# Kernel tuning notes

Measured on AMD Instinct MI355X. Metric: run time of the kernel, lower is better.

The kernel has to match this reference:

```python
import jax, jax.numpy as jnp
import numpy as np
from jax import lax

M_DIM = 128
L1 = L2 = L3 = L4 = 4
L = L1 * L2 * L3 * L4  # 256
RANK = 2
BATCH, D = 4, 16
W = D - RANK + 1  # 15 windows per dim (linear mode, stride 1, drop)


def _make_bbasis():
    # Bbasis[idx, i] = prod_d cos(2*pi*(j_d+1)/(i+2)), idx = ((j1*L2+j2)*L3+j3)*L4+j4
    i = jnp.arange(M_DIM, dtype=jnp.float32)
    def c(Ld):
        j = jnp.arange(D_ := Ld, dtype=jnp.float32)
        return jnp.cos(2.0 * jnp.pi * (j[:, None] + 1.0) / (i[None, :] + 2.0))  # (Ld, m)
    B1, B2, B3, B4 = c(L1), c(L2), c(L3), c(L4)
    Bb = (B1[:, None, None, None, :] * B2[None, :, None, None, :]
          * B3[None, None, :, None, :] * B4[None, None, None, :, :])
    return Bb.reshape(L, M_DIM).astype(jnp.float32)


def setup_inputs() -> dict:
    key = jax.random.key(0)
    k1, k2, k3 = jax.random.split(key, 3)
    vec_arr = jax.random.normal(k1, (BATCH, D, D, D, D, M_DIM), dtype=jnp.float32)
    # M initialized as identity + small noise (nn.init.eye_ is exactly eye; noise keeps grads non-trivial)
    M = jnp.eye(M_DIM, dtype=jnp.float32) + 0.01 * jax.random.normal(k2, (M_DIM, M_DIM), dtype=jnp.float32)
    Acoeff = jax.random.uniform(k3, (M_DIM, L), minval=-0.1, maxval=0.1, dtype=jnp.float32)
    Bbasis = _make_bbasis()
    return {"vec_arr": vec_arr, "M": M, "Acoeff": Acoeff, "Bbasis": Bbasis}


def _basis_index():
    # window coords k_d in [0, W), basis index uses j_d = k_d mod L_d
    k = jnp.arange(W)
    j1 = (k % L1)[:, None, None, None]
    j2 = (k % L2)[None, :, None, None]
    j3 = (k % L3)[None, None, :, None]
    j4 = (k % L4)[None, None, None, :]
    idx = ((j1 * L2 + j2) * L3 + j3) * L4 + j4  # (W,W,W,W)
    return idx.reshape(-1)  # (W^4,)


def reference(vec_arr, M, Acoeff, Bbasis):
    # 4D sliding-window mean (linear mode, stride 1, 'drop'), rank_op='avg'.
    # mean(window @ M.T) == mean(window) @ M.T (linearity), so pool then one GEMM.
    win = (1, RANK, RANK, RANK, RANK, 1)
    pooled = lax.reduce_window(vec_arr, jnp.float32(0.0), lax.add, win,
                               (1, 1, 1, 1, 1, 1), 'VALID') / float(RANK ** 4)
    # agg[b, k1..k4, j] = sum_i pooled[...,i] * M[j,i]  (i.e. x @ M.T)
    agg = jnp.einsum('bwxyzi,ji->bwxyzj', pooled, M)  # (B, W,W,W,W, m)
    agg = agg.reshape(agg.shape[0], -1, M_DIM)        # (B, W^4, m)
    idx = _basis_index()                               # (W^4,)
    # Position-dependent descriptor N(k) = Acoeff[:, idx] * Bbasis[idx, :]
    Nk = Acoeff.T[idx] * Bbasis[idx]                   # (W^4, m)
    return Nk[None, :, :] - agg                        # (B, W^4, m) deviation
```

## Files before the change

kernel.cpp:

```cpp
#include <hip/hip_runtime.h>
#include <hip/hip_bf16.h>
#include <stdint.h>

#define MD     128
#define W4     50625
#define ROWS   202500
#define LBAS   256
#define POOL_THREADS 432000
#define NK_OFF 51840000

typedef __attribute__((ext_vector_type(8))) __bf16 bf16x8;
typedef __attribute__((ext_vector_type(4))) float floatx4;
typedef __attribute__((ext_vector_type(8))) unsigned short ushortx8;
typedef __attribute__((ext_vector_type(4))) unsigned short ushortx4;

__device__ __forceinline__ float bf2f(unsigned short u){
  union { unsigned int i; float f; } v; v.i = ((unsigned int)u) << 16; return v.f;
}
__device__ __forceinline__ unsigned short f2bf(float x){
  union { float f; unsigned int i; } v; v.f = x;
  unsigned int r = v.i + 0x7FFFu + ((v.i >> 16) & 1u);
  return (unsigned short)(r >> 16);
}
__device__ __forceinline__ int detect_f32(const void* Bbasis){
  return ((const unsigned int*)Bbasis)[0] == 0x3F800000u;
}

__global__ __launch_bounds__(256) void nk_kernel(const void* __restrict__ Acoeff,
                                                 const void* __restrict__ Bbasis,
                                                 float* __restrict__ NkFull){
  int gid = blockIdx.x * 256 + threadIdx.x;
  if (gid >= LBAS * MD) return;
  int idx = gid >> 7;
  int j   = gid & 127;
  float a, b;
  if (detect_f32(Bbasis)){
    a = ((const float*)Acoeff)[j * LBAS + idx];
    b = ((const float*)Bbasis)[idx * MD + j];
  } else {
    a = bf2f(((const unsigned short*)Acoeff)[j * LBAS + idx]);
    b = bf2f(((const unsigned short*)Bbasis)[idx * MD + j]);
  }
  NkFull[gid] = a * b;
}

template<int ISF32>
__device__ __forceinline__ void pool_body(const void* __restrict__ vec,
                                          unsigned short* __restrict__ pooled,
                                          int gid){
  const int ig = gid & 31;
  unsigned int strip = (unsigned int)(gid >> 5);
  const unsigned int w4 = strip % 15u; strip /= 15u;
  const unsigned int w3 = strip % 15u; strip /= 15u;
  const unsigned int w2 = strip % 15u;
  const unsigned int b  = strip / 15u;
  const unsigned int base = b*8388608u + w2*32768u + w3*2048u + w4*128u
                          + (unsigned int)(ig * 4);
  unsigned int offs[8];
#pragma unroll
  for (int d = 0; d < 8; ++d){
    const unsigned int d2 = (d>>2)&1u, d3 = (d>>1)&1u, d4 = d&1u;
    offs[d] = base + d2*32768u + d3*2048u + d4*128u;
  }
  const unsigned int prowB = b*50625u + w2*225u + w3*15u + w4;
  float prev[4], cur[4];
#pragma unroll 4
  for (int k1 = 0; k1 < 16; ++k1){
#pragma unroll
    for (int e = 0; e < 4; ++e) cur[e] = 0.f;
#pragma unroll
    for (int d = 0; d < 8; ++d){
      const unsigned int off = offs[d] + (unsigned int)k1 * 524288u;
      if (ISF32){
        const floatx4 v = *(const floatx4*)((const float*)vec + off);
#pragma unroll
        for (int e = 0; e < 4; ++e) cur[e] += v[e];
      } else {
        const ushortx4 u = *(const ushortx4*)((const unsigned short*)vec + off);
#pragma unroll
        for (int e = 0; e < 4; ++e) cur[e] += bf2f(u[e]);
      }
    }
    if (k1 > 0){
      ushortx4 ov;
#pragma unroll
      for (int e = 0; e < 4; ++e) ov[e] = f2bf((prev[e] + cur[e]) * 0.0625f);
      *(ushortx4*)(pooled + (size_t)(prowB + (unsigned)(k1 - 1) * 3375u) * 128 + ig * 4) = ov;
    }
#pragma unroll
    for (int e = 0; e < 4; ++e) prev[e] = cur[e];
  }
}

__global__ __launch_bounds__(256) void pool_kernel(const void* __restrict__ vec,
                                                   const void* __restrict__ Bbasis,
                                                   unsigned short* __restrict__ pooled){
  int gid = blockIdx.x * 256 + threadIdx.x;
  if (gid >= POOL_THREADS) return;
  if (detect_f32(Bbasis)) pool_body<1>(vec, pooled, gid);
  else                    pool_body<0>(vec, pooled, gid);
}

union GemmSmem {
  struct { unsigned short A[128][136]; unsigned short B[128][136]; } ab;
  float C[128][132];
};

__global__ __launch_bounds__(256) void gemm_kernel(const unsigned short* __restrict__ pooled,
                                                   const void* __restrict__ Mmat,
                                                   const float* __restrict__ NkFull,
                                                   const void* __restrict__ Bbasis,
                                                   void* __restrict__ out){
  __shared__ __align__(16) GemmSmem sm;
  __shared__ int sIdx[128];

  const int tid = threadIdx.x;
  const int p0  = blockIdx.x * 128;
  const int isF32 = detect_f32(Bbasis);

  {
    const int rr  = tid >> 4;
    const int l16 = tid & 15;
#pragma unroll
    for (int r8 = 0; r8 < 8; ++r8){
      const int row = r8 * 16 + rr;
      *(ushortx8*)&sm.ab.A[row][l16 * 8] =
          *(const ushortx8*)(pooled + (size_t)(p0 + row) * 128 + l16 * 8);
    }
    if (isF32){
      const float* mf = (const float*)Mmat;
#pragma unroll
      for (int r8 = 0; r8 < 8; ++r8){
        const int row = r8 * 16 + rr;
        const float* src = mf + row * 128 + l16 * 8;
        floatx4 lo = *(const floatx4*)src;
        floatx4 hi = *(const floatx4*)(src + 4);
        ushortx8 v;
#pragma unroll
        for (int e = 0; e < 4; ++e){ v[e] = f2bf(lo[e]); v[4+e] = f2bf(hi[e]); }
        *(ushortx8*)&sm.ab.B[row][l16 * 8] = v;
      }
    } else {
      const unsigned short* mh = (const unsigned short*)Mmat;
#pragma unroll
      for (int r8 = 0; r8 < 8; ++r8){
        const int row = r8 * 16 + rr;
        *(ushortx8*)&sm.ab.B[row][l16 * 8] = *(const ushortx8*)(mh + row * 128 + l16 * 8);
      }
    }
  }
  if (tid < 128){
    const int p = p0 + tid;
    unsigned int w = (p < ROWS) ? (unsigned int)(p % W4) : 0u;
    const unsigned int w4 = w % 15u; w /= 15u;
    const unsigned int w3 = w % 15u; w /= 15u;
    const unsigned int w2 = w % 15u;
    const unsigned int w1 = w / 15u;
    sIdx[tid] = (int)(((w1 & 3u) << 6) | ((w2 & 3u) << 4) | ((w3 & 3u) << 2) | (w4 & 3u));
  }
  __syncthreads();

  const int wave = tid >> 6;
  const int lane = tid & 63;
  const int quad = lane >> 4;
  const int l16  = lane & 15;

  floatx4 acc[2][8];
#pragma unroll
  for (int rt = 0; rt < 2; ++rt)
#pragma unroll
    for (int c = 0; c < 8; ++c) acc[rt][c] = (floatx4){0.f, 0.f, 0.f, 0.f};

#pragma unroll
  for (int s = 0; s < 4; ++s){
    bf16x8 af[2];
#pragma unroll
    for (int rt = 0; rt < 2; ++rt)
      af[rt] = *(const bf16x8*)&sm.ab.A[wave * 32 + rt * 16 + l16][s * 32 + quad * 8];
#pragma unroll
    for (int c = 0; c < 8; ++c){
      const bf16x8 bfv = *(const bf16x8*)&sm.ab.B[c * 16 + l16][s * 32 + quad * 8];
      acc[0][c] = __builtin_amdgcn_mfma_f32_16x16x32_bf16(af[0], bfv, acc[0][c], 0, 0, 0);
      acc[1][c] = __builtin_amdgcn_mfma_f32_16x16x32_bf16(af[1], bfv, acc[1][c], 0, 0, 0);
    }
  }

  __syncthreads();
#pragma unroll
  for (int rt = 0; rt < 2; ++rt){
#pragma unroll
    for (int c = 0; c < 8; ++c){
#pragma unroll
      for (int reg = 0; reg < 4; ++reg){
        const int r = wave * 32 + rt * 16 + quad * 4 + reg;
        sm.C[r][c * 16 + l16] = acc[rt][c][reg];
      }
    }
  }
  __syncthreads();

  const int rsub = tid >> 5;
  const int col  = (tid & 31) * 4;
#pragma unroll
  for (int k = 0; k < 16; ++k){
    const int row = k * 8 + rsub;
    const int p = p0 + row;
    if (p >= ROWS) continue;
    const floatx4 v = *(const floatx4*)&sm.C[row][col];
    const floatx4 nk = *(const floatx4*)(NkFull + (sIdx[row] << 7) + col);
    floatx4 o;
#pragma unroll
    for (int e = 0; e < 4; ++e) o[e] = nk[e] - v[e];
    if (isF32){
      *(floatx4*)((float*)out + (size_t)p * 128 + col) = o;
    } else {
      ushortx4 ob;
#pragma unroll
      for (int e = 0; e < 4; ++e) ob[e] = f2bf(o[e]);
      *(ushortx4*)((unsigned short*)out + (size_t)p * 128 + col) = ob;
    }
  }
}

extern "C" void kernel_launch(void* const* d_in, const int* in_sizes, int n_in,
                              void* d_out, int out_size, void* d_ws, size_t ws_size,
                              hipStream_t stream) {
  const void* vec = d_in[0];
  const void* Mm  = d_in[1];
  const void* Ac  = d_in[2];
  const void* Bb  = d_in[3];

  unsigned short* pooled = (unsigned short*)d_ws;
  float* NkFull = (float*)((char*)d_ws + NK_OFF);

  nk_kernel<<<128, 256, 0, stream>>>(Ac, Bb, NkFull);
  pool_kernel<<<(POOL_THREADS + 255) / 256, 256, 0, stream>>>(vec, Bb, pooled);
  gemm_kernel<<<(ROWS + 127) / 128, 256, 0, stream>>>(pooled, Mm, NkFull, Bb, d_out);
}
```

Baseline: 283.9 us.

## Split 4D pooling into separable passes fused with GEMM and Nk epilogue

Replaces the per-thread 16-load pooling with a separable scheme. Pass A reads pairs of slices along dim2, sums them in shared memory and does the dim3/dim4 2x2 pooling, writing a partially pooled bf16 buffer. Pass B finishes the dim1 pair sum while loading the GEMM A tile, then runs the MFMA GEMM with a Nk tile cached in shared memory and a pre-converted bf16 M. The goal is less redundant reading of the large input and cheaper staging of M and Nk, in exchange for an extra intermediate buffer written and read through global memory, double bf16 rounding, and a dependence on the workspace being large enough.

New measurement: 267.9 us. 1.06x faster.

```diff
diff --git a/kernel.cpp b/kernel.cpp
--- a/kernel.cpp
+++ b/kernel.cpp
@@ -6,8 +6,15 @@
 #define W4     50625
 #define ROWS   202500
 #define LBAS   256
+
+#define P_ELEMS  27648000ull
+#define P_BYTES  (P_ELEMS*2ull)
+#define NK2_OFF  P_BYTES
+#define MBF_OFF  (P_BYTES + 131072ull)
+#define WS_NEED  (P_BYTES + 131072ull + 32768ull)
+
+#define NK_OFF 51840000
 #define POOL_THREADS 432000
-#define NK_OFF 51840000
 
 typedef __attribute__((ext_vector_type(8))) __bf16 bf16x8;
 typedef __attribute__((ext_vector_type(4))) float floatx4;
@@ -24,6 +31,219 @@
 }
 __device__ __forceinline__ int detect_f32(const void* Bbasis){
   return ((const unsigned int*)Bbasis)[0] == 0x3F800000u;
+}
+
+__global__ __launch_bounds__(256) void nk2_kernel(const void* __restrict__ Acoeff,
+                                                  const void* __restrict__ Bbasis,
+                                                  const void* __restrict__ Mmat,
+                                                  float* __restrict__ NkFull,
+                                                  unsigned short* __restrict__ Mbf){
+  int gid = blockIdx.x * 256 + threadIdx.x;
+  const int isf = detect_f32(Bbasis);
+  if (gid < LBAS * MD){
+    int idx = gid >> 7, j = gid & 127;
+    float a, b;
+    if (isf){ a = ((const float*)Acoeff)[j*LBAS+idx]; b = ((const float*)Bbasis)[idx*MD+j]; }
+    else    { a = bf2f(((const unsigned short*)Acoeff)[j*LBAS+idx]);
+              b = bf2f(((const unsigned short*)Bbasis)[idx*MD+j]); }
+    NkFull[gid] = a * b;
+  } else {
+    int m = gid - LBAS * MD;
+    if (m < MD * MD){
+      Mbf[m] = isf ? f2bf(((const float*)Mmat)[m]) : ((const unsigned short*)Mmat)[m];
+    }
+  }
+}
+
+__global__ __launch_bounds__(256) void passA_kernel(const void* __restrict__ vec,
+                                                    const void* __restrict__ Bbasis,
+                                                    unsigned short* __restrict__ P){
+  __shared__ __align__(16) float S[256 * 68];
+
+  const int bid = blockIdx.x;
+  const int l   = (bid & 7) * 240 + (bid >> 3);
+  const int w2  = l % 15;
+  int r = l / 15;
+  const int ih  = r & 1;  r >>= 1;
+  const int x1  = r & 15;
+  const int b   = r >> 4;
+  const int t   = threadIdx.x;
+
+  const size_t baseA = ((size_t)((b * 16 + x1) * 16 + w2)) * 32768 + (size_t)ih * 64;
+  const size_t baseB = baseA + 32768;
+  const int isf = detect_f32(Bbasis);
+
+  if (isf){
+    const float* vf = (const float*)vec;
+#pragma unroll
+    for (int k = 0; k < 16; ++k){
+      const int e   = k * 1024 + t * 4;
+      const size_t off = (size_t)(e >> 6) * 128 + (e & 63);
+      const floatx4 a = *(const floatx4*)(vf + baseA + off);
+      const floatx4 c = *(const floatx4*)(vf + baseB + off);
+      floatx4 s;
+#pragma unroll
+      for (int q = 0; q < 4; ++q) s[q] = a[q] + c[q];
+      *(floatx4*)&S[(e >> 6) * 68 + (e & 63)] = s;
+    }
+  } else {
+    const unsigned short* vh = (const unsigned short*)vec;
+#pragma unroll
+    for (int k = 0; k < 16; ++k){
+      const int e   = k * 1024 + t * 4;
+      const size_t off = (size_t)(e >> 6) * 128 + (e & 63);
+      const ushortx4 a = *(const ushortx4*)(vh + baseA + off);
+      const ushortx4 c = *(const ushortx4*)(vh + baseB + off);
+      floatx4 s;
+#pragma unroll
+      for (int q = 0; q < 4; ++q) s[q] = bf2f(a[q]) + bf2f(c[q]);
+      *(floatx4*)&S[(e >> 6) * 68 + (e & 63)] = s;
+    }
+  }
+  __syncthreads();
+
+  const int ig = t & 7;
+  const int wp = t >> 3;
+  unsigned short* Pbase = P + ((size_t)((b * 16 + x1) * 15 + w2)) * 28800 + ih * 64 + ig * 8;
+#pragma unroll
+  for (int j = 0; j < 8; ++j){
+    const int w34 = j * 32 + wp;
+    if (w34 < 225){
+      const int w3 = w34 / 15;
+      const int w4 = w34 - w3 * 15;
+      const int p00 = (w3 * 16 + w4) * 68 + ig * 8;
+      const float* r00 = &S[p00];
+      const float* r01 = &S[p00 + 68];
+      const float* r10 = &S[p00 + 68 * 16];
+      const float* r11 = &S[p00 + 68 * 17];
+      ushortx8 ov;
+#pragma unroll
+      for (int e = 0; e < 8; ++e){
+        const float s = (r00[e] + r01[e]) + (r10[e] + r11[e]);
+        ov[e] = f2bf(s * 0.125f);
+      }
+      *(ushortx8*)(Pbase + (size_t)w34 * 128) = ov;
+    }
+  }
+}
+
+__global__ __launch_bounds__(256) void passB_kernel(const unsigned short* __restrict__ P,
+                                                    const float* __restrict__ NkFull,
+                                                    const unsigned short* __restrict__ Mbf,
+                                                    const void* __restrict__ Bbasis,
+                                                    void* __restrict__ out){
+  __shared__ __align__(16) unsigned short sAp[128][136];
+  __shared__ __align__(16) unsigned short sB[128][136];
+  __shared__ __align__(16) float sNk[16 * 128];
+  __shared__ unsigned char sJ[128];
+
+  const int bid = blockIdx.x;
+  const int l   = (bid % 8) * 225 + (bid / 8);
+  const int half = l & 1;
+  int s2 = l >> 1;
+  const int w2 = s2 % 15;  s2 /= 15;
+  const int w1 = s2 % 15;
+  const int b  = s2 / 15;
+  const int r0 = half * 128;
+  const int RN = half ? 97 : 128;
+  const int t  = threadIdx.x;
+  const int isf = detect_f32(Bbasis);
+
+  {
+    const int rr  = t >> 4;
+    const int l16 = t & 15;
+    const size_t sb0 = ((size_t)((b * 16 + w1) * 15 + w2)) * 28800;
+    const size_t sb1 = sb0 + 432000;
+#pragma unroll
+    for (int it = 0; it < 8; ++it){
+      const int row = it * 16 + rr;
+      const size_t off = (size_t)(r0 + row) * 128 + l16 * 8;
+      const ushortx8 u0 = *(const ushortx8*)(P + sb0 + off);
+      const ushortx8 u1 = *(const ushortx8*)(P + sb1 + off);
+      ushortx8 sv;
+#pragma unroll
+      for (int e = 0; e < 8; ++e) sv[e] = f2bf((bf2f(u0[e]) + bf2f(u1[e])) * 0.5f);
+      *(ushortx8*)&sAp[row][l16 * 8] = sv;
+      *(ushortx8*)&sB[row][l16 * 8] = *(const ushortx8*)(Mbf + row * 128 + l16 * 8);
+    }
+  }
+  {
+    const int nkbase = ((w1 & 3) * 4 + (w2 & 3)) * 16;
+    const floatx4 n0 = *(const floatx4*)(NkFull + nkbase * 128 + t * 8);
+    const floatx4 n1 = *(const floatx4*)(NkFull + nkbase * 128 + t * 8 + 4);
+    *(floatx4*)&sNk[t * 8]     = n0;
+    *(floatx4*)&sNk[t * 8 + 4] = n1;
+  }
+  if (t < 128){
+    const int w34 = r0 + t;
+    if (w34 < 225){
+      const int w3 = w34 / 15;
+      const int w4 = w34 - w3 * 15;
+      sJ[t] = (unsigned char)((w3 & 3) * 4 + (w4 & 3));
+    } else sJ[t] = 0;
+  }
+  __syncthreads();
+
+  const int wave = t >> 6;
+  const int lane = t & 63;
+  const int quad = lane >> 4;
+  const int l16m = lane & 15;
+
+  floatx4 acc[2][8];
+#pragma unroll
+  for (int rt = 0; rt < 2; ++rt)
+#pragma unroll
+    for (int c = 0; c < 8; ++c) acc[rt][c] = (floatx4){0.f, 0.f, 0.f, 0.f};
+
+#pragma unroll
+  for (int s = 0; s < 4; ++s){
+    const bf16x8 af0 = *(const bf16x8*)&sAp[wave * 16 + l16m][s * 32 + quad * 8];
+    const bf16x8 af1 = *(const bf16x8*)&sAp[64 + wave * 16 + l16m][s * 32 + quad * 8];
+#pragma unroll
+    for (int c = 0; c < 8; ++c){
+      const bf16x8 bfv = *(const bf16x8*)&sB[c * 16 + l16m][s * 32 + quad * 8];
+      acc[0][c] = __builtin_amdgcn_mfma_f32_16x16x32_bf16(af0, bfv, acc[0][c], 0, 0, 0);
+      acc[1][c] = __builtin_amdgcn_mfma_f32_16x16x32_bf16(af1, bfv, acc[1][c], 0, 0, 0);
+    }
+  }
+  __syncthreads();
+
+  float* Ct = (float*)&sB[0][0];
+  const size_t prow0 = ((size_t)((b * 15 + w1) * 15 + w2)) * 225 + r0;
+
+#pragma unroll
+  for (int s = 0; s < 2; ++s){
+#pragma unroll
+    for (int c = 0; c < 8; ++c)
+#pragma unroll
+      for (int reg = 0; reg < 4; ++reg)
+        Ct[(wave * 16 + quad * 4 + reg) * 132 + c * 16 + l16m] = acc[s][c][reg];
+    __syncthreads();
+
+    const int col = (t & 31) * 4;
+#pragma unroll
+    for (int k = 0; k < 8; ++k){
+      const int lr = k * 8 + (t >> 5);
+      const int rloc = 64 * s + lr;
+      if (rloc < RN){
+        const floatx4 v  = *(const floatx4*)&Ct[lr * 132 + col];
+        const floatx4 nk = *(const floatx4*)&sNk[(int)sJ[rloc] * 128 + col];
+        floatx4 o;
+#pragma unroll
+        for (int e = 0; e < 4; ++e) o[e] = nk[e] - v[e];
+        const size_t p = prow0 + rloc;
+        if (isf){
+          *(floatx4*)((float*)out + p * 128 + col) = o;
+        } else {
+          ushortx4 ob;
+#pragma unroll
+          for (int e = 0; e < 4; ++e) ob[e] = f2bf(o[e]);
+          *(ushortx4*)((unsigned short*)out + p * 128 + col) = ob;
+        }
+      }
+    }
+    if (s == 0) __syncthreads();
+  }
 }
 
 __global__ __launch_bounds__(256) void nk_kernel(const void* __restrict__ Acoeff,
@@ -31,8 +251,7 @@
                                                  float* __restrict__ NkFull){
   int gid = blockIdx.x * 256 + threadIdx.x;
   if (gid >= LBAS * MD) return;
-  int idx = gid >> 7;
-  int j   = gid & 127;
+  int idx = gid >> 7, j = gid & 127;
   float a, b;
   if (detect_f32(Bbasis)){
     a = ((const float*)Acoeff)[j * LBAS + idx];
@@ -230,10 +449,18 @@
   const void* Ac  = d_in[2];
   const void* Bb  = d_in[3];
 
-  unsigned short* pooled = (unsigned short*)d_ws;
-  float* NkFull = (float*)((char*)d_ws + NK_OFF);
-
-  nk_kernel<<<128, 256, 0, stream>>>(Ac, Bb, NkFull);
-  pool_kernel<<<(POOL_THREADS + 255) / 256, 256, 0, stream>>>(vec, Bb, pooled);
-  gemm_kernel<<<(ROWS + 127) / 128, 256, 0, stream>>>(pooled, Mm, NkFull, Bb, d_out);
-}
+  if (ws_size >= WS_NEED){
+    unsigned short* P = (unsigned short*)d_ws;
+    float* NkFull = (float*)((char*)d_ws + NK2_OFF);
+    unsigned short* Mbf = (unsigned short*)((char*)d_ws + MBF_OFF);
+    nk2_kernel<<<192, 256, 0, stream>>>(Ac, Bb, Mm, NkFull, Mbf);
+    passA_kernel<<<1920, 256, 0, stream>>>(vec, Bb, P);
+    passB_kernel<<<1800, 256, 0, stream>>>(P, NkFull, Mbf, Bb, d_out);
+  } else {
+    unsigned short* pooled = (unsigned short*)d_ws;
+    float* NkFull = (float*)((char*)d_ws + NK_OFF);
+    nk_kernel<<<128, 256, 0, stream>>>(Ac, Bb, NkFull);
+    pool_kernel<<<(POOL_THREADS + 255) / 256, 256, 0, stream>>>(vec, Bb, pooled);
+    gemm_kernel<<<(ROWS + 127) / 128, 256, 0, stream>>>(pooled, Mm, NkFull, Bb, d_out);
+  }
+}
```

## Fuse pooling, GEMM and epilogue into one streaming kernel per (b,w2,w3) strip

Applied to the files above, without the earlier changes.

Replaces the separate pool and GEMM kernels with a single kernel in which each block owns one (batch, w2, w3) strip and streams over x1. It sums slices in shared memory, keeps the previous pooled slice in a ring buffer, runs a small MFMA GEMM against M held in LDS, and writes the output directly. This removes the pooled intermediate round-trip through global memory and one kernel launch, and pre-converts M to bf16 once. The cost is that only 900 blocks run, each with serial x1 steps and several barriers, and the pooled values are now rounded to bf16 twice.

New measurement: 250.0 us. 12.0% less time.

```diff
diff --git a/kernel.cpp b/kernel.cpp
--- a/kernel.cpp
+++ b/kernel.cpp
@@ -2,12 +2,11 @@
 #include <hip/hip_bf16.h>
 #include <stdint.h>
 
-#define MD     128
-#define W4     50625
-#define ROWS   202500
-#define LBAS   256
-#define POOL_THREADS 432000
-#define NK_OFF 51840000
+#define MD   128
+#define LBAS 256
+
+#define MBF_OFF 131072ull
+#define WS_NEED (131072ull + 32768ull)
 
 typedef __attribute__((ext_vector_type(8))) __bf16 bf16x8;
 typedef __attribute__((ext_vector_type(4))) float floatx4;
@@ -26,198 +25,212 @@
   return ((const unsigned int*)Bbasis)[0] == 0x3F800000u;
 }
 
-__global__ __launch_bounds__(256) void nk_kernel(const void* __restrict__ Acoeff,
-                                                 const void* __restrict__ Bbasis,
-                                                 float* __restrict__ NkFull){
+__global__ __launch_bounds__(256) void nk2_kernel(const void* __restrict__ Acoeff,
+                                                  const void* __restrict__ Bbasis,
+                                                  const void* __restrict__ Mmat,
+                                                  float* __restrict__ NkFull,
+                                                  unsigned short* __restrict__ Mbf){
   int gid = blockIdx.x * 256 + threadIdx.x;
-  if (gid >= LBAS * MD) return;
-  int idx = gid >> 7;
-  int j   = gid & 127;
-  float a, b;
-  if (detect_f32(Bbasis)){
-    a = ((const float*)Acoeff)[j * LBAS + idx];
-    b = ((const float*)Bbasis)[idx * MD + j];
+  const int isf = detect_f32(Bbasis);
+  if (gid < LBAS * MD){
+    int idx = gid >> 7, j = gid & 127;
+    float a, b;
+    if (isf){ a = ((const float*)Acoeff)[j*LBAS+idx]; b = ((const float*)Bbasis)[idx*MD+j]; }
+    else    { a = bf2f(((const unsigned short*)Acoeff)[j*LBAS+idx]);
+              b = bf2f(((const unsigned short*)Bbasis)[idx*MD+j]); }
+    NkFull[gid] = a * b;
   } else {
-    a = bf2f(((const unsigned short*)Acoeff)[j * LBAS + idx]);
-    b = bf2f(((const unsigned short*)Bbasis)[idx * MD + j]);
-  }
-  NkFull[gid] = a * b;
-}
-
-template<int ISF32>
-__device__ __forceinline__ void pool_body(const void* __restrict__ vec,
-                                          unsigned short* __restrict__ pooled,
-                                          int gid){
-  const int ig = gid & 31;
-  unsigned int strip = (unsigned int)(gid >> 5);
-  const unsigned int w4 = strip % 15u; strip /= 15u;
-  const unsigned int w3 = strip % 15u; strip /= 15u;
-  const unsigned int w2 = strip % 15u;
-  const unsigned int b  = strip / 15u;
-  const unsigned int base = b*8388608u + w2*32768u + w3*2048u + w4*128u
-                          + (unsigned int)(ig * 4);
-  unsigned int offs[8];
-#pragma unroll
-  for (int d = 0; d < 8; ++d){
-    const unsigned int d2 = (d>>2)&1u, d3 = (d>>1)&1u, d4 = d&1u;
-    offs[d] = base + d2*32768u + d3*2048u + d4*128u;
-  }
-  const unsigned int prowB = b*50625u + w2*225u + w3*15u + w4;
-  float prev[4], cur[4];
-#pragma unroll 4
-  for (int k1 = 0; k1 < 16; ++k1){
-#pragma unroll
-    for (int e = 0; e < 4; ++e) cur[e] = 0.f;
-#pragma unroll
-    for (int d = 0; d < 8; ++d){
-      const unsigned int off = offs[d] + (unsigned int)k1 * 524288u;
-      if (ISF32){
-        const floatx4 v = *(const floatx4*)((const float*)vec + off);
-#pragma unroll
-        for (int e = 0; e < 4; ++e) cur[e] += v[e];
+    int m = gid - LBAS * MD;
+    if (m < MD * MD){
+      Mbf[m] = isf ? f2bf(((const float*)Mmat)[m]) : ((const unsigned short*)Mmat)[m];
+    }
+  }
+}
+
+__global__ __launch_bounds__(256, 2) void mega_kernel(const void* __restrict__ vec,
+                                                      const float* __restrict__ NkFull,
+                                                      const unsigned short* __restrict__ Mbf,
+                                                      const void* __restrict__ Bbasis,
+                                                      void* __restrict__ out){
+  __shared__ __align__(16) float S[32 * 132];
+  __shared__ __align__(16) unsigned short Mb[128][136];
+  __shared__ __align__(16) unsigned short pp[2][15][136];
+  __shared__ __align__(16) unsigned short Ab[16 * 136];
+  __shared__ __align__(16) float sNkStep[512];
+
+  const int xcd  = blockIdx.x & 7;
+  const int slot = blockIdx.x >> 3;
+  const int b    = xcd >> 1;
+  const int s    = slot * 2 + (xcd & 1);
+  if (s >= 225) return;
+  const int w3 = s / 15;
+  const int w2 = s - w3 * 15;
+  const int t  = threadIdx.x;
+  const int isf = detect_f32(Bbasis);
+
+#pragma unroll
+  for (int k = 0; k < 8; ++k){
+    const int f = k * 256 + t;
+    const int row = f >> 4, c8 = (f & 15) * 8;
+    *(ushortx8*)&Mb[row][c8] = *(const ushortx8*)(Mbf + row * 128 + c8);
+  }
+
+  const size_t vbase0 = (size_t)b * 8388608 + (size_t)w2 * 32768 + (size_t)w3 * 2048;
+
+  int offF[4];
+#pragma unroll
+  for (int k = 0; k < 4; ++k){
+    const int ci = k * 256 + t;
+    const int row = ci >> 5;
+    offF[k] = (row >> 4) * 2048 + (row & 15) * 128 + (ci & 31) * 4;
+  }
+  int offB[2];
+#pragma unroll
+  for (int k = 0; k < 2; ++k){
+    const int ci = k * 256 + t;
+    const int row = ci >> 4;
+    offB[k] = (row >> 4) * 2048 + (row & 15) * 128 + (ci & 15) * 8;
+  }
+
+  floatx4 pre[4][2];
+
+  if (isf){
+    const float* vf = (const float*)vec + vbase0;
+#pragma unroll
+    for (int k = 0; k < 4; ++k){
+      pre[k][0] = *(const floatx4*)(vf + offF[k]);
+      pre[k][1] = *(const floatx4*)(vf + offF[k] + 32768);
+    }
+  } else {
+    const unsigned short* vh = (const unsigned short*)vec + vbase0;
+#pragma unroll
+    for (int k = 0; k < 2; ++k){
+      *(ushortx8*)&pre[k][0] = *(const ushortx8*)(vh + offB[k]);
+      *(ushortx8*)&pre[k][1] = *(const ushortx8*)(vh + offB[k] + 32768);
+    }
+  }
+
+  const int pw4 = t >> 4;
+  const int pc8 = (t & 15) * 8;
+  const int wave = t >> 6, lane = t & 63;
+  const int quad = lane >> 4, l16 = lane & 15;
+
+  for (int x1 = 0; x1 < 16; ++x1){
+    __syncthreads();
+
+    if (isf){
+#pragma unroll
+      for (int k = 0; k < 4; ++k){
+        const int ci = k * 256 + t;
+        const int row = ci >> 5, c4 = (ci & 31) * 4;
+        floatx4 sv;
+#pragma unroll
+        for (int q = 0; q < 4; ++q) sv[q] = pre[k][0][q] + pre[k][1][q];
+        *(floatx4*)&S[row * 132 + c4] = sv;
+      }
+    } else {
+#pragma unroll
+      for (int k = 0; k < 2; ++k){
+        const int ci = k * 256 + t;
+        const int row = ci >> 4, c8 = (ci & 15) * 8;
+        const ushortx8 a = *(const ushortx8*)&pre[k][0];
+        const ushortx8 c = *(const ushortx8*)&pre[k][1];
+#pragma unroll
+        for (int q = 0; q < 8; ++q) S[row * 132 + c8 + q] = bf2f(a[q]) + bf2f(c[q]);
+      }
+    }
+
+    if (x1 < 15){
+      if (isf){
+        const float* vf = (const float*)vec + vbase0 + (size_t)(x1 + 1) * 524288;
+#pragma unroll
+        for (int k = 0; k < 4; ++k){
+          pre[k][0] = *(const floatx4*)(vf + offF[k]);
+          pre[k][1] = *(const floatx4*)(vf + offF[k] + 32768);
+        }
       } else {
-        const ushortx4 u = *(const ushortx4*)((const unsigned short*)vec + off);
-#pragma unroll
-        for (int e = 0; e < 4; ++e) cur[e] += bf2f(u[e]);
-      }
-    }
-    if (k1 > 0){
-      ushortx4 ov;
-#pragma unroll
-      for (int e = 0; e < 4; ++e) ov[e] = f2bf((prev[e] + cur[e]) * 0.0625f);
-      *(ushortx4*)(pooled + (size_t)(prowB + (unsigned)(k1 - 1) * 3375u) * 128 + ig * 4) = ov;
-    }
-#pragma unroll
-    for (int e = 0; e < 4; ++e) prev[e] = cur[e];
-  }
-}
-
-__global__ __launch_bounds__(256) void pool_kernel(const void* __restrict__ vec,
-                                                   const void* __restrict__ Bbasis,
-                                                   unsigned short* __restrict__ pooled){
-  int gid = blockIdx.x * 256 + threadIdx.x;
-  if (gid >= POOL_THREADS) return;
-  if (detect_f32(Bbasis)) pool_body<1>(vec, pooled, gid);
-  else                    pool_body<0>(vec, pooled, gid);
-}
-
-union GemmSmem {
-  struct { unsigned short A[128][136]; unsigned short B[128][136]; } ab;
-  float C[128][132];
-};
-
-__global__ __launch_bounds__(256) void gemm_kernel(const unsigned short* __restrict__ pooled,
-                                                   const void* __restrict__ Mmat,
-                                                   const float* __restrict__ NkFull,
-                                                   const void* __restrict__ Bbasis,
-                                                   void* __restrict__ out){
-  __shared__ __align__(16) GemmSmem sm;
-  __shared__ int sIdx[128];
-
-  const int tid = threadIdx.x;
-  const int p0  = blockIdx.x * 128;
-  const int isF32 = detect_f32(Bbasis);
-
-  {
-    const int rr  = tid >> 4;
-    const int l16 = tid & 15;
-#pragma unroll
-    for (int r8 = 0; r8 < 8; ++r8){
-      const int row = r8 * 16 + rr;
-      *(ushortx8*)&sm.ab.A[row][l16 * 8] =
-          *(const ushortx8*)(pooled + (size_t)(p0 + row) * 128 + l16 * 8);
-    }
-    if (isF32){
-      const float* mf = (const float*)Mmat;
-#pragma unroll
-      for (int r8 = 0; r8 < 8; ++r8){
-        const int row = r8 * 16 + rr;
-        const float* src = mf + row * 128 + l16 * 8;
-        floatx4 lo = *(const floatx4*)src;
-        floatx4 hi = *(const floatx4*)(src + 4);
-        ushortx8 v;
-#pragma unroll
-        for (int e = 0; e < 4; ++e){ v[e] = f2bf(lo[e]); v[4+e] = f2bf(hi[e]); }
-        *(ushortx8*)&sm.ab.B[row][l16 * 8] = v;
-      }
-    } else {
-      const unsigned short* mh = (const unsigned short*)Mmat;
-#pragma unroll
-      for (int r8 = 0; r8 < 8; ++r8){
-        const int row = r8 * 16 + rr;
-        *(ushortx8*)&sm.ab.B[row][l16 * 8] = *(const ushortx8*)(mh + row * 128 + l16 * 8);
-      }
-    }
-  }
-  if (tid < 128){
-    const int p = p0 + tid;
-    unsigned int w = (p < ROWS) ? (unsigned int)(p % W4) : 0u;
-    const unsigned int w4 = w % 15u; w /= 15u;
-    const unsigned int w3 = w % 15u; w /= 15u;
-    const unsigned int w2 = w % 15u;
-    const unsigned int w1 = w / 15u;
-    sIdx[tid] = (int)(((w1 & 3u) << 6) | ((w2 & 3u) << 4) | ((w3 & 3u) << 2) | (w4 & 3u));
-  }
-  __syncthreads();
-
-  const int wave = tid >> 6;
-  const int lane = tid & 63;
-  const int quad = lane >> 4;
-  const int l16  = lane & 15;
-
-  floatx4 acc[2][8];
-#pragma unroll
-  for (int rt = 0; rt < 2; ++rt)
-#pragma unroll
-    for (int c = 0; c < 8; ++c) acc[rt][c] = (floatx4){0.f, 0.f, 0.f, 0.f};
-
-#pragma unroll
-  for (int s = 0; s < 4; ++s){
-    bf16x8 af[2];
-#pragma unroll
-    for (int rt = 0; rt < 2; ++rt)
-      af[rt] = *(const bf16x8*)&sm.ab.A[wave * 32 + rt * 16 + l16][s * 32 + quad * 8];
-#pragma unroll
-    for (int c = 0; c < 8; ++c){
-      const bf16x8 bfv = *(const bf16x8*)&sm.ab.B[c * 16 + l16][s * 32 + quad * 8];
-      acc[0][c] = __builtin_amdgcn_mfma_f32_16x16x32_bf16(af[0], bfv, acc[0][c], 0, 0, 0);
-      acc[1][c] = __builtin_amdgcn_mfma_f32_16x16x32_bf16(af[1], bfv, acc[1][c], 0, 0, 0);
-    }
-  }
-
-  __syncthreads();
-#pragma unroll
-  for (int rt = 0; rt < 2; ++rt){
-#pragma unroll
-    for (int c = 0; c < 8; ++c){
-#pragma unroll
-      for (int reg = 0; reg < 4; ++reg){
-        const int r = wave * 32 + rt * 16 + quad * 4 + reg;
-        sm.C[r][c * 16 + l16] = acc[rt][c][reg];
-      }
-    }
-  }
-  __syncthreads();
-
-  const int rsub = tid >> 5;
-  const int col  = (tid & 31) * 4;
-#pragma unroll
-  for (int k = 0; k < 16; ++k){
-    const int row = k * 8 + rsub;
-    const int p = p0 + row;
-    if (p >= ROWS) continue;
-    const floatx4 v = *(const floatx4*)&sm.C[row][col];
-    const floatx4 nk = *(const floatx4*)(NkFull + (sIdx[row] << 7) + col);
-    floatx4 o;
-#pragma unroll
-    for (int e = 0; e < 4; ++e) o[e] = nk[e] - v[e];
-    if (isF32){
-      *(floatx4*)((float*)out + (size_t)p * 128 + col) = o;
-    } else {
-      ushortx4 ob;
-#pragma unroll
-      for (int e = 0; e < 4; ++e) ob[e] = f2bf(o[e]);
-      *(ushortx4*)((unsigned short*)out + (size_t)p * 128 + col) = ob;
+        const unsigned short* vh = (const unsigned short*)vec + vbase0 + (size_t)(x1 + 1) * 524288;
+#pragma unroll
+        for (int k = 0; k < 2; ++k){
+          *(ushortx8*)&pre[k][0] = *(const ushortx8*)(vh + offB[k]);
+          *(ushortx8*)&pre[k][1] = *(const ushortx8*)(vh + offB[k] + 32768);
+        }
+      }
+    }
+    __syncthreads();
+
+    const int cb = x1 & 1, pbuf = cb ^ 1;
+    if (t < 240){
+      float cur[8];
+      const int p0 = pw4 * 132 + pc8;
+#pragma unroll
+      for (int e = 0; e < 8; ++e)
+        cur[e] = ((S[p0 + e] + S[p0 + 132 + e]) +
+                  (S[p0 + 16 * 132 + e] + S[p0 + 17 * 132 + e])) * 0.125f;
+      ushortx8 cv;
+#pragma unroll
+      for (int e = 0; e < 8; ++e) cv[e] = f2bf(cur[e]);
+      *(ushortx8*)&pp[cb][pw4][pc8] = cv;
+      if (x1 > 0){
+        const ushortx8 pv = *(const ushortx8*)&pp[pbuf][pw4][pc8];
+        ushortx8 av;
+#pragma unroll
+        for (int e = 0; e < 8; ++e) av[e] = f2bf((cur[e] + bf2f(pv[e])) * 0.5f);
+        *(ushortx8*)&Ab[pw4 * 136 + pc8] = av;
+      }
+    }
+    __syncthreads();
+
+    if (x1 > 0){
+      floatx4 acc[2];
+      acc[0] = (floatx4){0.f,0.f,0.f,0.f};
+      acc[1] = (floatx4){0.f,0.f,0.f,0.f};
+#pragma unroll
+      for (int s4 = 0; s4 < 4; ++s4){
+        const bf16x8 af = *(const bf16x8*)&Ab[l16 * 136 + s4 * 32 + quad * 8];
+#pragma unroll
+        for (int cc = 0; cc < 2; ++cc){
+          const bf16x8 bv = *(const bf16x8*)&Mb[(wave * 2 + cc) * 16 + l16][s4 * 32 + quad * 8];
+          acc[cc] = __builtin_amdgcn_mfma_f32_16x16x32_bf16(af, bv, acc[cc], 0, 0, 0);
+        }
+      }
+      float* Ct = S;
+#pragma unroll
+      for (int cc = 0; cc < 2; ++cc)
+#pragma unroll
+        for (int reg = 0; reg < 4; ++reg)
+          Ct[(quad * 4 + reg) * 132 + (wave * 2 + cc) * 16 + l16] = acc[cc][reg];
+
+      const int j1 = (x1 - 1) & 3;
+      const int idxBase = ((j1 * 4 + (w2 & 3)) * 4 + (w3 & 3)) * 4;
+#pragma unroll
+      for (int k = 0; k < 2; ++k){
+        const int e = k * 256 + t;
+        sNkStep[e] = NkFull[(idxBase + (e >> 7)) * 128 + (e & 127)];
+      }
+      __syncthreads();
+
+      const size_t outBase = ((size_t)(((b * 15 + (x1 - 1)) * 15 + w2) * 15 + w3)) * 15;
+#pragma unroll
+      for (int k = 0; k < 2; ++k){
+        const int ci = k * 256 + t;
+        if (ci < 480){
+          const int row = ci >> 5, c4 = (ci & 31) * 4;
+          const floatx4 v  = *(const floatx4*)&Ct[row * 132 + c4];
+          const floatx4 nk = *(const floatx4*)&sNkStep[(row & 3) * 128 + c4];
+          floatx4 o;
+#pragma unroll
+          for (int e = 0; e < 4; ++e) o[e] = nk[e] - v[e];
+          if (isf){
+            *(floatx4*)((float*)out + (outBase + row) * 128 + c4) = o;
+          } else {
+            ushortx4 ob;
+#pragma unroll
+            for (int e = 0; e < 4; ++e) ob[e] = f2bf(o[e]);
+            *(ushortx4*)((unsigned short*)out + (outBase + row) * 128 + c4) = ob;
+          }
+        }
+      }
     }
   }
 }
@@ -230,10 +243,9 @@
   const void* Ac  = d_in[2];
   const void* Bb  = d_in[3];
 
-  unsigned short* pooled = (unsigned short*)d_ws;
-  float* NkFull = (float*)((char*)d_ws + NK_OFF);
-
-  nk_kernel<<<128, 256, 0, stream>>>(Ac, Bb, NkFull);
-  pool_kernel<<<(POOL_THREADS + 255) / 256, 256, 0, stream>>>(vec, Bb, pooled);
-  gemm_kernel<<<(ROWS + 127) / 128, 256, 0, stream>>>(pooled, Mm, NkFull, Bb, d_out);
-}
+  float* NkFull = (float*)d_ws;
+  unsigned short* Mbf = (unsigned short*)((char*)d_ws + MBF_OFF);
+
+  nk2_kernel<<<192, 256, 0, stream>>>(Ac, Bb, Mm, NkFull, Mbf);
+  mega_kernel<<<904, 256, 0, stream>>>(vec, NkFull, Mbf, Bb, d_out);
+}
```
